# Optimization experiments

Measured on AMD Instinct MI355X. Metric: run time of the kernel, lower is better.

The kernel has to match this reference:

```python
import jax, jax.numpy as jnp
import numpy as np

KERNEL_SIZE = 5  # convolution kernel size (number of past true events per query time)


def _temporal_enc(dt, in_channels):
    # dt: (...,) -> (..., in_channels) sinusoidal encoding, matching __temporal_enc
    i = jnp.arange(in_channels)
    pos = jnp.power(10000.0, 2.0 * (i // 2).astype(jnp.float32) / in_channels)
    r = dt[..., None] / pos
    return jnp.where(i % 2 == 0, jnp.sin(r), jnp.cos(r))


def _forward(times, true_times, true_features, non_pad_mask, sim_size, W1, b1, W2, b2):
    K = KERNEL_SIZE
    bs, L = true_times.shape
    C = true_features.shape[-1]
    OUT = W2.shape[1] // C
    s = int(sim_size)
    pad = K - 1
    mask = non_pad_mask.astype(bool)

    # conv1d-with-identity-kernel == sliding window of the K past events (left zero pad)
    tt = jnp.pad(true_times, ((0, 0), (pad, 0)))
    tf = jnp.pad(true_features, ((0, 0), (pad, 0), (0, 0)))
    mm = jnp.pad(mask, ((0, 0), (pad, 0)))
    idx = jnp.arange(K)[:, None] + jnp.arange(L)[None, :]  # (K, L)
    pct = tt[:, idx]                      # (bs, K, L) windowed true times
    pcf = tf[:, idx, :]                   # (bs, K, L, C) windowed features
    dm = mm[:, idx] & mask[:, None, :]    # (bs, K, L) valid-pair mask

    # expand over simulated times: repeat each slot (sim_size+1) times along L
    Lall = (s + 1) * L - s                # == (sim_size+1)*(L-1)+1
    pct = jnp.repeat(pct, s + 1, axis=2)[:, :, :Lall]          # trim last s
    pcf = jnp.repeat(pcf, s + 1, axis=2)[:, :, :Lall, :]       # trim last s
    dm = jnp.repeat(dm, s + 1, axis=2)[:, :, s:]               # trim FIRST s (as in torch code)

    dt = times[:, None, :] - pct                                # (bs, K, Lall)
    dt = jnp.where(dm, dt, 0.0)
    pcf = jnp.where(dm[..., None], pcf, 0.0)                    # (bs, K, Lall, C)

    # temporal encoding + kernel MLP; zero out masked positions (masked-gather semantics)
    te = _temporal_enc(dt, C) * dm[..., None]                   # (bs, K, Lall, C)
    h = jax.nn.relu(te @ W1 + b1)                               # (bs, K, Lall, H)
    kv = (h @ W2 + b2).reshape(bs, K, Lall, C, OUT)
    kv = kv * dm[..., None, None]

    # elementwise multiply + reduce over kernel slots and in_channels
    out = jnp.einsum('bklc,bklco->blo', pcf, kv)                # (bs, Lall, OUT)
    return out


def setup_inputs() -> dict:
    key = jax.random.key(0)
    ks = jax.random.split(key, 8)
    bs, L, C, OUT, H, s = 8, 256, 32, 32, 16, 5
    Lall = (s + 1) * (L - 1) + 1  # 1531
    return {
        'times': jax.random.uniform(ks[0], (bs, Lall), dtype=jnp.float32),
        'true_times': jax.random.uniform(ks[1], (bs, L), dtype=jnp.float32),
        'true_features': jax.random.normal(ks[2], (bs, L, C), dtype=jnp.float32),
        'non_pad_mask': jnp.ones((bs, L), dtype=bool),
        'sim_size': s,
        'W1': jax.random.normal(ks[3], (C, H), dtype=jnp.float32) / np.sqrt(C),
        'b1': jnp.zeros((H,), dtype=jnp.float32),
        'W2': jax.random.normal(ks[4], (H, C * OUT), dtype=jnp.float32) / np.sqrt(H),
        'b2': jnp.zeros((C * OUT,), dtype=jnp.float32),
    }


def reference(times, true_times, true_features, non_pad_mask, sim_size, W1, b1, W2, b2):
    return _forward(times, true_times, true_features, non_pad_mask, sim_size, W1, b1, W2, b2)
```

## Files before the change

### kernel.cpp

```cpp
#include <hip/hip_runtime.h>

#define BS   8
#define LEN  256
#define CCH  32
#define OUTC 32
#define HID  16
#define SS   5
#define KK   5
#define LALL ((SS + 1) * LEN - SS)
#define LPB  4
#define NROW (LPB + KK - 1)
#define NCH  (LPB * 6 * KK)
#define TES  33

__global__ __launch_bounds__(256) void fused_kernel(
        const float* __restrict__ times, const float* __restrict__ true_times,
        const float* __restrict__ tf,    const int* __restrict__ mask,
        const float* __restrict__ W1,    const float* __restrict__ b1,
        const float* __restrict__ W2,    const float* __restrict__ b2,
        float* __restrict__ out) {
    const int l0  = blockIdx.x * LPB;
    const int b   = blockIdx.y;
    const int tid = threadIdx.x;

    __shared__ float sQ[NROW][HID * OUTC];
    __shared__ float sPb[NROW][OUTC];
    __shared__ float sF[NROW][CCH];
    __shared__ float sW1[CCH * HID];
    __shared__ float sb1[HID];
    __shared__ float sPT[NROW];
    __shared__ float sM[NROW + 1];
    __shared__ float sT[LPB * 6];
    __shared__ float sInv[16];
    __shared__ float sTE[NCH * TES];
    __shared__ float sH[NCH * HID];

    for (int e = tid; e < CCH * HID; e += 256) sW1[e] = W1[e];
    if (tid < HID) sb1[tid] = b1[tid];
    if (tid < 16) sInv[tid] = __powf(10000.f, -(float)tid * (1.f / 16.f));
    if (tid < NROW * CCH) {
        int ri = tid >> 5, c = tid & 31;
        int row = l0 + ri - (KK - 1);
        sF[ri][c] = (row >= 0) ? tf[(size_t)(b * LEN + row) * CCH + c] : 0.f;
    }
    if (tid < NROW) {
        int row = l0 + tid - (KK - 1);
        sPT[tid] = (row >= 0) ? true_times[b * LEN + row] : 0.f;
    }
    if (tid >= 32 && tid < 32 + NROW + 1) {
        int i = tid - 32;
        int row = l0 + i - (KK - 1);
        int rc = row < (LEN - 1) ? row : (LEN - 1);
        sM[i] = (row >= 0 && mask[b * LEN + rc] != 0) ? 1.f : 0.f;
    }
    if (tid >= 64 && tid < 64 + LPB * 6) {
        int jl = tid - 64;
        int j = 6 * l0 + jl;
        sT[jl] = (j < LALL) ? times[(size_t)b * LALL + j] : 0.f;
    }
    __syncthreads();

    {
        int o = tid & 31;
        int h0 = tid >> 5;
        int h1 = (tid + 256) >> 5;
        const float* w0 = W2 + (size_t)h0 * (CCH * OUTC) + o;
        const float* w1 = W2 + (size_t)h1 * (CCH * OUTC) + o;
        float acc0[NROW], acc1[NROW];
#pragma unroll
        for (int r = 0; r < NROW; ++r) { acc0[r] = 0.f; acc1[r] = 0.f; }
#pragma unroll
        for (int c = 0; c < CCH; ++c) {
            float wv0 = w0[c * OUTC];
            float wv1 = w1[c * OUTC];
#pragma unroll
            for (int r = 0; r < NROW; ++r) {
                float fv = sF[r][c];
                acc0[r] += fv * wv0;
                acc1[r] += fv * wv1;
            }
        }
#pragma unroll
        for (int r = 0; r < NROW; ++r) {
            sQ[r][tid]       = acc0[r];
            sQ[r][tid + 256] = acc1[r];
        }
    }
    {
        int ri = tid >> 5, o = tid & 31;
        float acc = 0.f;
#pragma unroll
        for (int c = 0; c < CCH; ++c) acc += sF[ri][c] * b2[c * OUTC + o];
        sPb[ri][o] = acc;
    }
    for (int e = tid; e < NCH * CCH; e += 256) {
        int c  = e & 31;
        int k  = (e >> 5) % KK;
        int jl = e / (KK * CCH);
        int il = jl / 6;
        float dt = sT[jl] - sPT[il + k];
        float r = dt * sInv[c >> 1];
        sTE[(jl * KK + k) * TES + c] = (c & 1) ? __cosf(r) : __sinf(r);
    }
    __syncthreads();

    for (int e = tid; e < NCH * HID; e += 256) {
        int hh = e & 15;
        int ch = e >> 4;
        const float* te = &sTE[ch * TES];
        float acc = sb1[hh];
#pragma unroll
        for (int c = 0; c < CCH; ++c) acc += te[c] * sW1[c * HID + hh];
        sH[ch * HID + hh] = acc > 0.f ? acc : 0.f;
    }
    __syncthreads();

    for (int e = tid; e < LPB * 6 * OUTC; e += 256) {
        int o  = e & 31;
        int jr = (e >> 5) % 6;
        int il = e / (6 * OUTC);
        int j = 6 * (l0 + il) + jr;
        if (j < LALL) {
            int sel = jr > 0 ? 1 : 0;
            float mlm = sM[il + sel + (KK - 1)];
            float acc = 0.f;
#pragma unroll
            for (int k = 0; k < KK; ++k) {
                float dmv = sM[il + sel + k] * mlm;
                int ri = il + k;
                const float* hp = &sH[((il * 6 + jr) * KK + k) * HID];
                const float* qp = &sQ[ri][o];
                float a2 = sPb[ri][o];
#pragma unroll
                for (int hh = 0; hh < HID; ++hh) a2 += hp[hh] * qp[hh * OUTC];
                acc += dmv * a2;
            }
            out[((size_t)b * LALL + j) * OUTC + o] = acc;
        }
    }
}

extern "C" void kernel_launch(void* const* d_in, const int* in_sizes, int n_in,
                              void* d_out, int out_size, void* d_ws, size_t ws_size,
                              hipStream_t stream) {
    const float* times      = (const float*)d_in[0];
    const float* true_times = (const float*)d_in[1];
    const float* tf         = (const float*)d_in[2];
    const int*   mask       = (const int*)d_in[3];
    const float* W1         = (const float*)d_in[5];
    const float* b1         = (const float*)d_in[6];
    const float* W2         = (const float*)d_in[7];
    const float* b2         = (const float*)d_in[8];
    float* out = (float*)d_out;

    fused_kernel<<<dim3(LEN / LPB, BS), 256, 0, stream>>>(
        times, true_times, tf, mask, W1, b1, W2, b2, out);
}
```

Before: 82.75 us.

## Double rows per block and fuse temporal encoding into per-thread hidden MLP

Raises the number of query rows per block from 4 to 8, which halves the grid and spreads the W2 projection of feature rows over more outputs. The temporal encoding is no longer staged in shared memory. Each of the 240 threads now computes sincos for its own (query, slot) pair and runs the 32x16 first MLP layer in registers, which removes one barrier and the sTE buffer. The cost is more register pressure, leaving 16 threads idle in that phase, and a smaller grid of 256 blocks, which may leave many CUs underused.

```diff
diff --git a/kernel.cpp b/kernel.cpp
--- a/kernel.cpp
+++ b/kernel.cpp
@@ -8,10 +8,9 @@
 #define SS   5
 #define KK   5
 #define LALL ((SS + 1) * LEN - SS)
-#define LPB  4
+#define LPB  8
 #define NROW (LPB + KK - 1)
 #define NCH  (LPB * 6 * KK)
-#define TES  33
 
 __global__ __launch_bounds__(256) void fused_kernel(
         const float* __restrict__ times, const float* __restrict__ true_times,
@@ -32,17 +31,16 @@
     __shared__ float sM[NROW + 1];
     __shared__ float sT[LPB * 6];
     __shared__ float sInv[16];
-    __shared__ float sTE[NCH * TES];
     __shared__ float sH[NCH * HID];
 
     for (int e = tid; e < CCH * HID; e += 256) sW1[e] = W1[e];
-    if (tid < HID) sb1[tid] = b1[tid];
-    if (tid < 16) sInv[tid] = __powf(10000.f, -(float)tid * (1.f / 16.f));
-    if (tid < NROW * CCH) {
-        int ri = tid >> 5, c = tid & 31;
+    for (int e = tid; e < NROW * CCH; e += 256) {
+        int ri = e >> 5, c = e & 31;
         int row = l0 + ri - (KK - 1);
         sF[ri][c] = (row >= 0) ? tf[(size_t)(b * LEN + row) * CCH + c] : 0.f;
     }
+    if (tid < HID) sb1[tid] = b1[tid];
+    if (tid < 16) sInv[tid] = __powf(10000.f, -(float)tid * (1.f / 16.f));
     if (tid < NROW) {
         int row = l0 + tid - (KK - 1);
         sPT[tid] = (row >= 0) ? true_times[b * LEN + row] : 0.f;
@@ -86,32 +84,36 @@
             sQ[r][tid + 256] = acc1[r];
         }
     }
-    {
-        int ri = tid >> 5, o = tid & 31;
+    for (int e = tid; e < NROW * OUTC; e += 256) {
+        int ri = e >> 5, o = e & 31;
         float acc = 0.f;
 #pragma unroll
         for (int c = 0; c < CCH; ++c) acc += sF[ri][c] * b2[c * OUTC + o];
         sPb[ri][o] = acc;
     }
-    for (int e = tid; e < NCH * CCH; e += 256) {
-        int c  = e & 31;
-        int k  = (e >> 5) % KK;
-        int jl = e / (KK * CCH);
+    if (tid < NCH) {
+        int k  = tid % KK;
+        int jl = tid / KK;
         int il = jl / 6;
         float dt = sT[jl] - sPT[il + k];
-        float r = dt * sInv[c >> 1];
-        sTE[(jl * KK + k) * TES + c] = (c & 1) ? __cosf(r) : __sinf(r);
-    }
-    __syncthreads();
-
-    for (int e = tid; e < NCH * HID; e += 256) {
-        int hh = e & 15;
-        int ch = e >> 4;
-        const float* te = &sTE[ch * TES];
-        float acc = sb1[hh];
+        float te[CCH];
 #pragma unroll
-        for (int c = 0; c < CCH; ++c) acc += te[c] * sW1[c * HID + hh];
-        sH[ch * HID + hh] = acc > 0.f ? acc : 0.f;
+        for (int i = 0; i < 16; ++i) {
+            float r = dt * sInv[i];
+            __sincosf(r, &te[2 * i], &te[2 * i + 1]);
+        }
+        float hacc[HID];
+#pragma unroll
+        for (int hh = 0; hh < HID; ++hh) hacc[hh] = sb1[hh];
+#pragma unroll
+        for (int c = 0; c < CCH; ++c) {
+            float tv = te[c];
+#pragma unroll
+            for (int hh = 0; hh < HID; ++hh) hacc[hh] += tv * sW1[c * HID + hh];
+        }
+#pragma unroll
+        for (int hh = 0; hh < HID; ++hh)
+            sH[tid * HID + hh] = hacc[hh] > 0.f ? hacc[hh] : 0.f;
     }
     __syncthreads();
 
```

Result: no change. 81.62 us (-1.4%).
